# Kernel optimization log

Hardware: AMD Instinct MI355X
Metric: run time of the kernel (lower is better)

The kernel has to match this reference:

```python
import jax, jax.numpy as jnp
import numpy as np

TOP_K = 2  # init top_k


def setup_inputs() -> dict:
    key = jax.random.key(0)
    ks = jax.random.split(key, 6)
    B, S, D, F, E = 4, 4096, 1024, 4096, 8
    return {
        "x": jax.random.normal(ks[0], (B, S, D), dtype=jnp.float32),
        "W_base": jax.random.normal(ks[1], (F, D), dtype=jnp.float32) * 0.02,
        "W_delta": jax.random.normal(ks[2], (F, D), dtype=jnp.float32) * 0.02,
        "bias": jax.random.normal(ks[3], (F,), dtype=jnp.float32) * 0.01,
        "alpha": jax.random.uniform(ks[4], (E,), dtype=jnp.float32),
        "beta": jax.random.uniform(ks[5], (E,), dtype=jnp.float32),
    }


def reference(x, W_base, W_delta, bias, alpha, beta):
    # Reconstructed per-expert encoder weight: W_e = alpha_e*W_base + beta_e*W_delta  [E,F,D]
    W = alpha[:, None, None] * W_base[None] + beta[:, None, None] * W_delta[None]
    mu_w = W.mean(axis=1)                 # column-wise mean   [E,D]
    var_w = W.var(axis=1)                 # biased variance    [E,D]
    bias_mean = bias.mean()
    # Fused batched stats: mu_h, sigma_h for all experts at once  [B,S,E]
    mu_h = jnp.einsum('bsd,ed->bse', x, mu_w) + bias_mean
    sigma_h = jnp.sqrt(jnp.einsum('bsd,ed->bse', x * x, var_w) + 1e-8)
    z = mu_h / (jnp.sqrt(jnp.asarray(2.0, x.dtype)) * sigma_h)
    router_logits = jax.lax.erf(z)        # sparsity scores    [B,S,E]
    # Top-k gating: softmax over top-k logits, scattered back to [B,S,E]
    top_v, top_i = jax.lax.top_k(router_logits, TOP_K)
    soft = jax.nn.softmax(top_v, axis=-1)                       # [B,S,K]
    onehot = jax.nn.one_hot(top_i, router_logits.shape[-1], dtype=soft.dtype)  # [B,S,K,E]
    router_weights = jnp.einsum('bsk,bske->bse', soft, onehot)
    return router_weights, router_logits
```

## Files before the change

kernel.cpp:

```cpp
#include <hip/hip_runtime.h>
#include <math.h>

#define DD 1024
#define FF 4096
#define NTOK 16384
#define NPART 256
#define FIN (NPART * 5 * DD)


template<int CTRL, int RMASK>
__device__ __forceinline__ float dppadd(float v) {
    int m = __builtin_amdgcn_update_dpp(0, __float_as_int(v), CTRL, RMASK, 0xF, false);
    return v + __int_as_float(m);
}
__device__ __forceinline__ float wave_sum64(float v) {
    v = dppadd<0x121, 0xF>(v);
    v = dppadd<0x122, 0xF>(v);
    v = dppadd<0x124, 0xF>(v);
    v = dppadd<0x128, 0xF>(v);
    v = dppadd<0x142, 0xA>(v);
    v = dppadd<0x143, 0xC>(v);
    return __int_as_float(__builtin_amdgcn_readlane(__float_as_int(v), 63));
}

__global__ __launch_bounds__(256) void stats1_kernel(
    const float* __restrict__ Wb, const float* __restrict__ Wd,
    float* __restrict__ ws)
{
    const int tx = threadIdx.x;
    const int ty = threadIdx.y;
    const int bx = blockIdx.x;
    const int by = blockIdx.y;
    const int c4 = bx * 64 + tx;

    const float4* Wb4 = (const float4*)Wb;
    const float4* Wd4 = (const float4*)Wd;

    float4 sb  = make_float4(0.f,0.f,0.f,0.f);
    float4 sd  = sb, sbb = sb, sdd = sb, sbd = sb;

    const int row0 = by * 16 + ty * 4;
    #pragma unroll
    for (int r = 0; r < 4; ++r) {
        const int row = row0 + r;
        float4 b = Wb4[row * 256 + c4];
        float4 d = Wd4[row * 256 + c4];
        sb.x += b.x; sb.y += b.y; sb.z += b.z; sb.w += b.w;
        sd.x += d.x; sd.y += d.y; sd.z += d.z; sd.w += d.w;
        sbb.x += b.x*b.x; sbb.y += b.y*b.y; sbb.z += b.z*b.z; sbb.w += b.w*b.w;
        sdd.x += d.x*d.x; sdd.y += d.y*d.y; sdd.z += d.z*d.z; sdd.w += d.w*d.w;
        sbd.x += b.x*d.x; sbd.y += b.y*d.y; sbd.z += b.z*d.z; sbd.w += b.w*d.w;
    }

    __shared__ float4 red[4][5][64];

    red[ty][0][tx] = sb;
    red[ty][1][tx] = sd;
    red[ty][2][tx] = sbb;
    red[ty][3][tx] = sdd;
    red[ty][4][tx] = sbd;
    __syncthreads();

    if (ty == 0) {
        #pragma unroll
        for (int k = 0; k < 5; ++k) {
            float4 acc = red[0][k][tx];
            #pragma unroll
            for (int g = 1; g < 4; ++g) {
                float4 a = red[g][k][tx];
                acc.x += a.x; acc.y += a.y; acc.z += a.z; acc.w += a.w;
            }
            ((float4*)(ws + by * (5 * DD) + k * DD))[c4] = acc;
        }
    }
}

__global__ __launch_bounds__(256) void stats2_kernel(
    const float* __restrict__ bias, float* __restrict__ ws)
{
    const int tid   = threadIdx.x;
    const int col   = tid & 15;
    const int slice = tid >> 4;
    const int c4    = blockIdx.x * 16 + col;

    const float4* p4 = (const float4*)ws;
    float4 acc = make_float4(0.f,0.f,0.f,0.f);
    #pragma unroll 4
    for (int p = slice * 16; p < slice * 16 + 16; ++p) {
        float4 a = p4[(size_t)p * 1280 + c4];
        acc.x += a.x; acc.y += a.y; acc.z += a.z; acc.w += a.w;
    }

    __shared__ float4 red[16][17];
    red[slice][col] = acc;
    __syncthreads();

    if (slice == 0) {
        float4 a = red[0][col];
        #pragma unroll
        for (int s = 1; s < 16; ++s) {
            float4 b = red[s][col];
            a.x += b.x; a.y += b.y; a.z += b.z; a.w += b.w;
        }
        ((float4*)(ws + FIN))[c4] = a;
    }

    if (blockIdx.x == 0) {
        float s = 0.f;
        #pragma unroll
        for (int i = 0; i < 16; ++i) s += bias[tid + 256 * i];
        #pragma unroll
        for (int off = 32; off > 0; off >>= 1) s += __shfl_xor(s, off);
        __shared__ float bws[4];
        if ((tid & 63) == 0) bws[tid >> 6] = s;
        __syncthreads();
        if (tid == 0) ws[FIN + 5120] = bws[0] + bws[1] + bws[2] + bws[3];
    }
}

__device__ __forceinline__ float sel2(int t, float a, float b) {
    return t ? b : a;
}

__global__ __launch_bounds__(256, 8) void router_kernel(
    const float* __restrict__ x,
    const float* __restrict__ alpha, const float* __restrict__ beta,
    const float* __restrict__ ws, float* __restrict__ out)
{
    __shared__ float4 smem[1280];
    float4* s_mb4 = smem;
    float4* s_md4 = smem + 256;
    float4* s_vb4 = smem + 512;
    float4* s_vd4 = smem + 768;
    float4* s_cb4 = smem + 1024;
    float* s_mb = (float*)s_mb4;
    float* s_md = (float*)s_md4;
    float* s_vb = (float*)s_vb4;
    float* s_vd = (float*)s_vd4;
    float* s_cb = (float*)s_cb4;

    const int tid  = threadIdx.x;
    const int lane = tid & 63;
    const int wave = tid >> 6;
    const int gw   = blockIdx.x * 4 + wave;
    const int tok0 = gw * 2;

    const float4* xr = (const float4*)(x) + (size_t)tok0 * 256;

    float4 xp0[2], xp1[2];
    #pragma unroll
    for (int t = 0; t < 2; ++t) xp0[t] = xr[t * 256 + 0 * 64 + lane];
    #pragma unroll
    for (int t = 0; t < 2; ++t) xp1[t] = xr[t * 256 + 1 * 64 + lane];

    const float invF = 1.0f / (float)FF;
    const float* fin = ws + FIN;

    for (int i = tid; i < DD; i += 256) {
        float sb  = fin[i];
        float sd  = fin[DD + i];
        float sbb = fin[2 * DD + i];
        float sdd = fin[3 * DD + i];
        float sbd = fin[4 * DD + i];
        float mb = sb * invF, md = sd * invF;
        s_mb[i] = mb;
        s_md[i] = md;
        s_vb[i] = fmaxf(sbb * invF - mb * mb, 0.f);
        s_vd[i] = fmaxf(sdd * invF - md * md, 0.f);
        s_cb[i] = sbd * invF - mb * md;
    }
    const float bias_mean = fin[5120] * invF;
    __syncthreads();

    float s1[2], s2[2], t1[2], t2[2], t3[2];
    #pragma unroll
    for (int t = 0; t < 2; ++t) { s1[t]=0.f; s2[t]=0.f; t1[t]=0.f; t2[t]=0.f; t3[t]=0.f; }

    #pragma unroll
    for (int it = 0; it < 4; ++it) {
        const int i4 = it * 64 + lane;
        const float4 mb = s_mb4[i4];
        const float4 md = s_md4[i4];
        const float4 vb = s_vb4[i4];
        const float4 vd = s_vd4[i4];
        const float4 cb = s_cb4[i4];
        #pragma unroll
        for (int t = 0; t < 2; ++t) {
            float4 xv = (it & 1) ? xp1[t] : xp0[t];
            float x2x = xv.x*xv.x, x2y = xv.y*xv.y, x2z = xv.z*xv.z, x2w = xv.w*xv.w;
            s1[t] += xv.x*mb.x + xv.y*mb.y + xv.z*mb.z + xv.w*mb.w;
            s2[t] += xv.x*md.x + xv.y*md.y + xv.z*md.z + xv.w*md.w;
            t1[t] += x2x*vb.x + x2y*vb.y + x2z*vb.z + x2w*vb.w;
            t2[t] += x2x*vd.x + x2y*vd.y + x2z*vd.z + x2w*vd.w;
            t3[t] += x2x*cb.x + x2y*cb.y + x2z*cb.z + x2w*cb.w;
        }
        if (it < 2) {
            #pragma unroll
            for (int t = 0; t < 2; ++t) {
                float4 nv = xr[t * 256 + (it + 2) * 64 + lane];
                if (it & 1) xp1[t] = nv; else xp0[t] = nv;
            }
        }
    }

    float A1[2], A2[2], B1[2], B2[2], B3[2];
    #pragma unroll
    for (int t = 0; t < 2; ++t) {
        A1[t] = wave_sum64(s1[t]);
        A2[t] = wave_sum64(s2[t]);
        B1[t] = wave_sum64(t1[t]);
        B2[t] = wave_sum64(t2[t]);
        B3[t] = wave_sum64(t3[t]);
    }

    const int tt = (lane >> 3) & 1;
    const int e  = lane & 7;
    const float a_e = alpha[e];
    const float b_e = beta[e];

    float S1 = sel2(tt, A1[0], A1[1]);
    float S2 = sel2(tt, A2[0], A2[1]);
    float T1 = sel2(tt, B1[0], B1[1]);
    float T2 = sel2(tt, B2[0], B2[1]);
    float T3 = sel2(tt, B3[0], B3[1]);

    float mu  = a_e * S1 + b_e * S2 + bias_mean;
    float var = a_e * a_e * T1 + b_e * b_e * T2 + 2.f * a_e * b_e * T3;
    float z   = mu / sqrtf(2.f * (var + 1e-8f));
    float logit = erff(z);

    const int base = lane & 56;
    float l[8];
    #pragma unroll
    for (int q = 0; q < 8; ++q) l[q] = __shfl(logit, base + q);

    float vmax = l[0]; int i0 = 0;
    #pragma unroll
    for (int q = 1; q < 8; ++q) { if (l[q] > vmax) { vmax = l[q]; i0 = q; } }
    float vsec = -1e30f; int i1 = 0;
    #pragma unroll
    for (int q = 0; q < 8; ++q) { if (q != i0 && l[q] > vsec) { vsec = l[q]; i1 = q; } }

    float e1  = __expf(vsec - vmax);
    float inv = 1.f / (1.f + e1);
    float wtop = inv, wsec = e1 * inv;

    if (lane < 16) {
        const int token = tok0 + tt;
        float w = (e == i0) ? wtop : ((e == i1) ? wsec : 0.f);
        out[(size_t)token * 8 + e] = w;
        out[(size_t)NTOK * 8 + (size_t)token * 8 + e] = logit;
    }
}

extern "C" void kernel_launch(void* const* d_in, const int* in_sizes, int n_in,
                              void* d_out, int out_size, void* d_ws, size_t ws_size,
                              hipStream_t stream)
{
    const float* x     = (const float*)d_in[0];
    const float* Wb    = (const float*)d_in[1];
    const float* Wd    = (const float*)d_in[2];
    const float* bias  = (const float*)d_in[3];
    const float* alpha = (const float*)d_in[4];
    const float* beta  = (const float*)d_in[5];
    float* out = (float*)d_out;
    float* ws  = (float*)d_ws;

    dim3 b1(64, 4), g1(4, 256);
    stats1_kernel<<<g1, b1, 0, stream>>>(Wb, Wd, ws);

    stats2_kernel<<<80, 256, 0, stream>>>(bias, ws);

    router_kernel<<<2048, 256, 0, stream>>>(x, alpha, beta, ws, out);
}
```

Measured before the change: 130.5 us.

## Use nontemporal loads and move final stats finalization into stats2

Streaming loads of W_base, W_delta and x now use nontemporal vector loads, so data read once is less likely to displace cached lines. stats2 is restructured to reduce all five stat arrays per column with a two-level shared reduction and to compute the final mean, variance and covariance once. Each router block then only copies the precomputed arrays into LDS, instead of all 2048 blocks repeating the finalization arithmetic. stats2 now runs 64 blocks with more serialized reduction work per block.

Result: slower. 136.6 us (+4.6%).

```diff
diff --git a/kernel.cpp b/kernel.cpp
--- a/kernel.cpp
+++ b/kernel.cpp
@@ -7,6 +7,12 @@
 #define NPART 256
 #define FIN (NPART * 5 * DD)
 
+
+typedef float fv4 __attribute__((ext_vector_type(4)));
+
+__device__ __forceinline__ fv4 ntload4(const void* p) {
+    return __builtin_nontemporal_load((const fv4*)p);
+}
 
 template<int CTRL, int RMASK>
 __device__ __forceinline__ float dppadd(float v) {
@@ -33,26 +39,26 @@
     const int by = blockIdx.y;
     const int c4 = bx * 64 + tx;
 
-    const float4* Wb4 = (const float4*)Wb;
-    const float4* Wd4 = (const float4*)Wd;
-
-    float4 sb  = make_float4(0.f,0.f,0.f,0.f);
-    float4 sd  = sb, sbb = sb, sdd = sb, sbd = sb;
+    const fv4* Wb4 = (const fv4*)Wb;
+    const fv4* Wd4 = (const fv4*)Wd;
+
+    fv4 sb  = {0.f,0.f,0.f,0.f};
+    fv4 sd = sb, sbb = sb, sdd = sb, sbd = sb;
 
     const int row0 = by * 16 + ty * 4;
     #pragma unroll
     for (int r = 0; r < 4; ++r) {
         const int row = row0 + r;
-        float4 b = Wb4[row * 256 + c4];
-        float4 d = Wd4[row * 256 + c4];
-        sb.x += b.x; sb.y += b.y; sb.z += b.z; sb.w += b.w;
-        sd.x += d.x; sd.y += d.y; sd.z += d.z; sd.w += d.w;
-        sbb.x += b.x*b.x; sbb.y += b.y*b.y; sbb.z += b.z*b.z; sbb.w += b.w*b.w;
-        sdd.x += d.x*d.x; sdd.y += d.y*d.y; sdd.z += d.z*d.z; sdd.w += d.w*d.w;
-        sbd.x += b.x*d.x; sbd.y += b.y*d.y; sbd.z += b.z*d.z; sbd.w += b.w*d.w;
-    }
-
-    __shared__ float4 red[4][5][64];
+        fv4 b = ntload4(&Wb4[row * 256 + c4]);
+        fv4 d = ntload4(&Wd4[row * 256 + c4]);
+        sb  += b;
+        sd  += d;
+        sbb += b * b;
+        sdd += d * d;
+        sbd += b * d;
+    }
+
+    __shared__ fv4 red[4][5][64];
 
     red[ty][0][tx] = sb;
     red[ty][1][tx] = sd;
@@ -64,13 +70,10 @@
     if (ty == 0) {
         #pragma unroll
         for (int k = 0; k < 5; ++k) {
-            float4 acc = red[0][k][tx];
+            fv4 acc = red[0][k][tx];
             #pragma unroll
-            for (int g = 1; g < 4; ++g) {
-                float4 a = red[g][k][tx];
-                acc.x += a.x; acc.y += a.y; acc.z += a.z; acc.w += a.w;
-            }
-            ((float4*)(ws + by * (5 * DD) + k * DD))[c4] = acc;
+            for (int g = 1; g < 4; ++g) acc += red[g][k][tx];
+            ((fv4*)(ws + by * (5 * DD) + k * DD))[c4] = acc;
         }
     }
 }
@@ -79,30 +82,69 @@
     const float* __restrict__ bias, float* __restrict__ ws)
 {
     const int tid   = threadIdx.x;
-    const int col   = tid & 15;
-    const int slice = tid >> 4;
-    const int c4    = blockIdx.x * 16 + col;
-
-    const float4* p4 = (const float4*)ws;
-    float4 acc = make_float4(0.f,0.f,0.f,0.f);
-    #pragma unroll 4
-    for (int p = slice * 16; p < slice * 16 + 16; ++p) {
-        float4 a = p4[(size_t)p * 1280 + c4];
-        acc.x += a.x; acc.y += a.y; acc.z += a.z; acc.w += a.w;
-    }
-
-    __shared__ float4 red[16][17];
-    red[slice][col] = acc;
+    const int col   = tid & 3;
+    const int slice = tid >> 2;
+    const int c4    = blockIdx.x * 4 + col;
+
+    const fv4* p4 = (const fv4*)ws;
+
+    __shared__ fv4 red [64][4][5];
+    __shared__ fv4 red2[ 8][4][5];
+
+    #pragma unroll
+    for (int k = 0; k < 5; ++k) {
+        fv4 acc = {0.f,0.f,0.f,0.f};
+        #pragma unroll
+        for (int j = 0; j < 4; ++j) {
+            const int p = slice * 4 + j;
+            acc += p4[(size_t)p * 1280 + k * 256 + c4];
+        }
+        red[slice][col][k] = acc;
+    }
     __syncthreads();
 
-    if (slice == 0) {
-        float4 a = red[0][col];
-        #pragma unroll
-        for (int s = 1; s < 16; ++s) {
-            float4 b = red[s][col];
-            a.x += b.x; a.y += b.y; a.z += b.z; a.w += b.w;
-        }
-        ((float4*)(ws + FIN))[c4] = a;
+    if (tid < 32) {
+        const int s8 = tid >> 2, c = tid & 3;
+        #pragma unroll
+        for (int k = 0; k < 5; ++k) {
+            fv4 a = red[s8 * 8 + 0][c][k];
+            #pragma unroll
+            for (int j = 1; j < 8; ++j) a += red[s8 * 8 + j][c][k];
+            red2[s8][c][k] = a;
+        }
+    }
+    __syncthreads();
+
+    if (tid < 4) {
+        const float invF = 1.0f / (float)FF;
+        fv4 f[5];
+        #pragma unroll
+        for (int k = 0; k < 5; ++k) {
+            fv4 a = red2[0][tid][k];
+            #pragma unroll
+            for (int s = 1; s < 8; ++s) a += red2[s][tid][k];
+            f[k] = a;
+        }
+        fv4 mb = f[0] * invF;
+        fv4 md = f[1] * invF;
+        fv4 vb, vd, cb;
+        vb.x = fmaxf(f[2].x * invF - mb.x*mb.x, 0.f);
+        vb.y = fmaxf(f[2].y * invF - mb.y*mb.y, 0.f);
+        vb.z = fmaxf(f[2].z * invF - mb.z*mb.z, 0.f);
+        vb.w = fmaxf(f[2].w * invF - mb.w*mb.w, 0.f);
+        vd.x = fmaxf(f[3].x * invF - md.x*md.x, 0.f);
+        vd.y = fmaxf(f[3].y * invF - md.y*md.y, 0.f);
+        vd.z = fmaxf(f[3].z * invF - md.z*md.z, 0.f);
+        vd.w = fmaxf(f[3].w * invF - md.w*md.w, 0.f);
+        cb = f[4] * invF - mb * md;
+
+        fv4* fin4 = (fv4*)(ws + FIN);
+        const int c = blockIdx.x * 4 + tid;
+        fin4[0 * 256 + c] = mb;
+        fin4[1 * 256 + c] = md;
+        fin4[2 * 256 + c] = vb;
+        fin4[3 * 256 + c] = vd;
+        fin4[4 * 256 + c] = cb;
     }
 
     if (blockIdx.x == 0) {
@@ -114,7 +156,8 @@
         __shared__ float bws[4];
         if ((tid & 63) == 0) bws[tid >> 6] = s;
         __syncthreads();
-        if (tid == 0) ws[FIN + 5120] = bws[0] + bws[1] + bws[2] + bws[3];
+        if (tid == 0)
+            ws[FIN + 5120] = (bws[0] + bws[1] + bws[2] + bws[3]) * (1.0f / (float)FF);
     }
 }
 
@@ -133,11 +176,6 @@
     float4* s_vb4 = smem + 512;
     float4* s_vd4 = smem + 768;
     float4* s_cb4 = smem + 1024;
-    float* s_mb = (float*)s_mb4;
-    float* s_md = (float*)s_md4;
-    float* s_vb = (float*)s_vb4;
-    float* s_vd = (float*)s_vd4;
-    float* s_cb = (float*)s_cb4;
 
     const int tid  = threadIdx.x;
     const int lane = tid & 63;
@@ -147,29 +185,16 @@
 
     const float4* xr = (const float4*)(x) + (size_t)tok0 * 256;
 
-    float4 xp0[2], xp1[2];
-    #pragma unroll
-    for (int t = 0; t < 2; ++t) xp0[t] = xr[t * 256 + 0 * 64 + lane];
-    #pragma unroll
-    for (int t = 0; t < 2; ++t) xp1[t] = xr[t * 256 + 1 * 64 + lane];
-
-    const float invF = 1.0f / (float)FF;
-    const float* fin = ws + FIN;
-
-    for (int i = tid; i < DD; i += 256) {
-        float sb  = fin[i];
-        float sd  = fin[DD + i];
-        float sbb = fin[2 * DD + i];
-        float sdd = fin[3 * DD + i];
-        float sbd = fin[4 * DD + i];
-        float mb = sb * invF, md = sd * invF;
-        s_mb[i] = mb;
-        s_md[i] = md;
-        s_vb[i] = fmaxf(sbb * invF - mb * mb, 0.f);
-        s_vd[i] = fmaxf(sdd * invF - md * md, 0.f);
-        s_cb[i] = sbd * invF - mb * md;
-    }
-    const float bias_mean = fin[5120] * invF;
+    fv4 xp0[2], xp1[2];
+    #pragma unroll
+    for (int t = 0; t < 2; ++t) xp0[t] = ntload4(&xr[t * 256 + 0 * 64 + lane]);
+    #pragma unroll
+    for (int t = 0; t < 2; ++t) xp1[t] = ntload4(&xr[t * 256 + 1 * 64 + lane]);
+
+    const float4* fin4 = (const float4*)(ws + FIN);
+    #pragma unroll
+    for (int i = 0; i < 5; ++i) smem[i * 256 + tid] = fin4[i * 256 + tid];
+    const float bias_mean = ws[FIN + 5120];
     __syncthreads();
 
     float s1[2], s2[2], t1[2], t2[2], t3[2];
@@ -186,7 +211,7 @@
         const float4 cb = s_cb4[i4];
         #pragma unroll
         for (int t = 0; t < 2; ++t) {
-            float4 xv = (it & 1) ? xp1[t] : xp0[t];
+            fv4 xv = (it & 1) ? xp1[t] : xp0[t];
             float x2x = xv.x*xv.x, x2y = xv.y*xv.y, x2z = xv.z*xv.z, x2w = xv.w*xv.w;
             s1[t] += xv.x*mb.x + xv.y*mb.y + xv.z*mb.z + xv.w*mb.w;
             s2[t] += xv.x*md.x + xv.y*md.y + xv.z*md.z + xv.w*md.w;
@@ -197,7 +222,7 @@
         if (it < 2) {
             #pragma unroll
             for (int t = 0; t < 2; ++t) {
-                float4 nv = xr[t * 256 + (it + 2) * 64 + lane];
+                fv4 nv = ntload4(&xr[t * 256 + (it + 2) * 64 + lane]);
                 if (it & 1) xp1[t] = nv; else xp0[t] = nv;
             }
         }
@@ -269,7 +294,7 @@
     dim3 b1(64, 4), g1(4, 256);
     stats1_kernel<<<g1, b1, 0, stream>>>(Wb, Wd, ws);
 
-    stats2_kernel<<<80, 256, 0, stream>>>(bias, ws);
+    stats2_kernel<<<64, 256, 0, stream>>>(bias, ws);
 
     router_kernel<<<2048, 256, 0, stream>>>(x, alpha, beta, ws, out);
 }
```
